# Kernel tuning notes

Hardware: AMD Instinct MI355X
Metric: run time of the kernel (lower is better)

Reference implementation:

```python
import jax, jax.numpy as jnp
import numpy as np

VOCAB = 100000
EMBED = 128
BATCH = 64
INPUT_LEN = 128
NB_WORDS = 50
RETAIN_P = 1.0  # dropout = 0.0


def setup_inputs() -> dict:
    key = jax.random.key(0)
    k1, k2 = jax.random.split(key)
    X = jax.random.randint(k1, (BATCH, INPUT_LEN, NB_WORDS), 0, VOCAB, dtype=jnp.int32)
    W = jax.random.normal(k2, (VOCAB, EMBED), dtype=jnp.float32)
    # original build() zeroes row 0 (padding row)
    W = W.at[0].set(0.0)
    return {"X": X, "W": W}


def reference(X, W):
    # inference path: B = ones(input_dim) * retain_p, so W_eff = W * retain_p
    # gather: (B, L, nb_words, E)
    emb = W[X] * RETAIN_P
    # zero-mask padding index 0, then bag-of-words sum over word axis
    mask = (X != 0).astype(emb.dtype)[..., None]
    out = jnp.sum(emb * mask, axis=2)  # (B, L, E)
    return out
```

## Files before the change

kernel.cpp:

```cpp
#include <hip/hip_runtime.h>
#include <hip/hip_bf16.h>


#define VOCAB     100000
#define EMBED     128
#define BATCH     64
#define INPUT_LEN 128
#define NB_WORDS  50
#define POSITIONS (BATCH * INPUT_LEN)

__global__ __launch_bounds__(256) void bag_embedding_kernel(
    const int* __restrict__ X,
    const float* __restrict__ W,
    float* __restrict__ out)
{
    const int gtid = blockIdx.x * blockDim.x + threadIdx.x;
    const int pos  = gtid >> 6;
    const int lane = threadIdx.x & 63;
    if (pos >= POSITIONS) return;

    const int* xp = X + pos * NB_WORDS;
    int myidx = (lane < NB_WORDS) ? xp[lane] : 0;

    const float2* __restrict__ W2 = (const float2*)W;
    float2 acc = make_float2(0.0f, 0.0f);

    #pragma unroll
    for (int w = 0; w < NB_WORDS; ++w) {
        int idx = __shfl(myidx, w);
        float2 v = W2[(size_t)idx * (EMBED / 2) + lane];
        acc.x += v.x;
        acc.y += v.y;
    }

    float2* o2 = (float2*)out;
    o2[(size_t)pos * (EMBED / 2) + lane] = acc;
}

extern "C" void kernel_launch(void* const* d_in, const int* in_sizes, int n_in,
                              void* d_out, int out_size, void* d_ws, size_t ws_size,
                              hipStream_t stream) {
    const int*   X = (const int*)d_in[0];
    const float* W = (const float*)d_in[1];
    float*     out = (float*)d_out;

    const int threads = 256;
    const int total   = POSITIONS * 64;
    const int blocks  = (total + threads - 1) / threads;
    bag_embedding_kernel<<<blocks, threads, 0, stream>>>(X, W, out);
}
```

Baseline: 104.6 us.

## Partition embedding gather by vocabulary range across blocks with a two-phase reduction

Splits the bag-of-words gather into 8 vocabulary ranges. Block index modulo 8 picks the range, so each block only gathers the rows of W whose indices fall inside its range and writes a partial sum to workspace. A second kernel sums the 8 partials into the output. The aim is to keep each group of blocks working on a smaller slice of W so the gathers hit in cache more often, which may line up with round-robin dispatch across XCDs. In exchange it adds about 64MB of workspace write and read traffic, a second kernel launch, and a serial ballot loop that has less memory-level parallelism than the fully unrolled loop.

```diff
diff --git a/kernel.cpp b/kernel.cpp
--- a/kernel.cpp
+++ b/kernel.cpp
@@ -8,8 +8,61 @@
 #define INPUT_LEN 128
 #define NB_WORDS  50
 #define POSITIONS (BATCH * INPUT_LEN)
+#define RANGES    8
+#define ROWS_PER_RANGE ((VOCAB + RANGES - 1) / RANGES)
 
-__global__ __launch_bounds__(256) void bag_embedding_kernel(
+__global__ __launch_bounds__(256) void bag_phase1(
+    const int* __restrict__ X,
+    const float* __restrict__ W,
+    float* __restrict__ ws)
+{
+    const int b     = blockIdx.x;
+    const int r     = b & (RANGES - 1);
+    const int chunk = b >> 3;
+    const int wave  = threadIdx.x >> 6;
+    const int lane  = threadIdx.x & 63;
+    const int pos   = chunk * 4 + wave;
+
+    const int lo = r * ROWS_PER_RANGE;
+    const int hi = (lo + ROWS_PER_RANGE < VOCAB) ? lo + ROWS_PER_RANGE : VOCAB;
+
+    const int* xp = X + pos * NB_WORDS;
+    int myidx = (lane < NB_WORDS) ? xp[lane] : -1;
+    bool inr = (lane < NB_WORDS) & (myidx >= lo) & (myidx < hi);
+    unsigned long long mask = __ballot(inr);
+
+    const float2* __restrict__ W2 = (const float2*)W;
+    float2 acc = make_float2(0.0f, 0.0f);
+
+    while (mask) {
+        int w = __ffsll((unsigned long long)mask) - 1;
+        mask &= mask - 1;
+        int idx = __builtin_amdgcn_readlane(myidx, w);
+        float2 v = W2[(size_t)idx * (EMBED / 2) + lane];
+        acc.x += v.x;
+        acc.y += v.y;
+    }
+
+    float2* o = (float2*)ws + ((size_t)r * POSITIONS + pos) * (EMBED / 2) + lane;
+    *o = acc;
+}
+
+__global__ __launch_bounds__(256) void bag_phase2(
+    const float* __restrict__ ws,
+    float* __restrict__ out)
+{
+    const int t = blockIdx.x * blockDim.x + threadIdx.x;
+    const float4* __restrict__ w4 = (const float4*)ws;
+    float4 s = make_float4(0.0f, 0.0f, 0.0f, 0.0f);
+    #pragma unroll
+    for (int r = 0; r < RANGES; ++r) {
+        float4 v = w4[(size_t)r * POSITIONS * (EMBED / 4) + t];
+        s.x += v.x; s.y += v.y; s.z += v.z; s.w += v.w;
+    }
+    ((float4*)out)[t] = s;
+}
+
+__global__ __launch_bounds__(256) void bag_onephase(
     const int* __restrict__ X,
     const float* __restrict__ W,
     float* __restrict__ out)
@@ -24,7 +77,6 @@
 
     const float2* __restrict__ W2 = (const float2*)W;
     float2 acc = make_float2(0.0f, 0.0f);
-
     #pragma unroll
     for (int w = 0; w < NB_WORDS; ++w) {
         int idx = __shfl(myidx, w);
@@ -32,7 +84,6 @@
         acc.x += v.x;
         acc.y += v.y;
     }
-
     float2* o2 = (float2*)out;
     o2[(size_t)pos * (EMBED / 2) + lane] = acc;
 }
@@ -44,8 +95,15 @@
     const float* W = (const float*)d_in[1];
     float*     out = (float*)d_out;
 
-    const int threads = 256;
-    const int total   = POSITIONS * 64;
-    const int blocks  = (total + threads - 1) / threads;
-    bag_embedding_kernel<<<blocks, threads, 0, stream>>>(X, W, out);
+    const size_t ws_needed = (size_t)RANGES * POSITIONS * EMBED * sizeof(float);
+    if (ws_size >= ws_needed) {
+        float* ws = (float*)d_ws;
+        bag_phase1<<<(POSITIONS / 4) * RANGES, 256, 0, stream>>>(X, W, ws);
+        bag_phase2<<<POSITIONS * (EMBED / 4) / 256, 256, 0, stream>>>(ws, out);
+    } else {
+        const int threads = 256;
+        const int total   = POSITIONS * 64;
+        const int blocks  = (total + threads - 1) / threads;
+        bag_onephase<<<blocks, threads, 0, stream>>>(X, W, out);
+    }
 }
```

After: 127.6 us. +22.0%, slower.

## Partition vocab into ranges per block for cache locality, reduce bf16 partials

Applied to the files above, without the earlier changes.

Splits the gather into two kernels. In the first, each block handles only words whose index falls in one of eight vocab ranges, aiming to keep that range's rows of W cache-resident, and it writes bf16-packed partial sums to a workspace. The second kernel sums the eight partials into fp32 output. This trades extra launches, the workspace traffic and bf16 rounding of the partials (a precision loss) for better reuse of W in cache. The new path runs only when the workspace is large enough, otherwise the old single-phase kernel is used.

```diff
diff --git a/kernel.cpp b/kernel.cpp
--- a/kernel.cpp
+++ b/kernel.cpp
@@ -1,5 +1,6 @@
 #include <hip/hip_runtime.h>
 #include <hip/hip_bf16.h>
+#include <stdint.h>
 
 
 #define VOCAB     100000
@@ -8,8 +9,77 @@
 #define INPUT_LEN 128
 #define NB_WORDS  50
 #define POSITIONS (BATCH * INPUT_LEN)
+#define RANGES    8
+#define ROWS_PER_RANGE (VOCAB / RANGES)
 
-__global__ __launch_bounds__(256) void bag_embedding_kernel(
+__device__ __forceinline__ uint32_t pack_bf16x2(float a, float b) {
+    uint32_t ua = __builtin_bit_cast(uint32_t, a);
+    uint32_t ub = __builtin_bit_cast(uint32_t, b);
+    uint32_t ra = (ua + 0x7fffu + ((ua >> 16) & 1u)) >> 16;
+    uint32_t rb = (ub + 0x7fffu + ((ub >> 16) & 1u)) >> 16;
+    return (rb << 16) | (ra & 0xffffu);
+}
+
+__global__ __launch_bounds__(256) void bag_phase1(
+    const int* __restrict__ X,
+    const float* __restrict__ W,
+    uint32_t* __restrict__ ws)
+{
+    const int b    = blockIdx.x;
+    const int r    = b & (RANGES - 1);
+    const int pos  = (b >> 3) * 4 + (threadIdx.x >> 6);
+    const int lane = threadIdx.x & 63;
+
+    const int lo = r * ROWS_PER_RANGE;
+    const int hi = lo + ROWS_PER_RANGE;
+
+    const int* xp = X + pos * NB_WORDS;
+    int myidx = (lane < NB_WORDS) ? xp[lane] : -1;
+    unsigned long long m = __ballot(myidx >= lo && myidx < hi);
+
+    const float2* __restrict__ W2 = (const float2*)W;
+    float2 acc = make_float2(0.0f, 0.0f);
+
+    while (m) {
+        int i0 = 0, i1 = 0, i2 = 0, i3 = 0;
+        {        int l = __ffsll(m) - 1; i0 = __builtin_amdgcn_readlane(myidx, l); m &= m - 1; }
+        if (m) { int l = __ffsll(m) - 1; i1 = __builtin_amdgcn_readlane(myidx, l); m &= m - 1; }
+        if (m) { int l = __ffsll(m) - 1; i2 = __builtin_amdgcn_readlane(myidx, l); m &= m - 1; }
+        if (m) { int l = __ffsll(m) - 1; i3 = __builtin_amdgcn_readlane(myidx, l); m &= m - 1; }
+        float2 v0 = W2[(size_t)i0 * (EMBED / 2) + lane];
+        float2 v1 = W2[(size_t)i1 * (EMBED / 2) + lane];
+        float2 v2 = W2[(size_t)i2 * (EMBED / 2) + lane];
+        float2 v3 = W2[(size_t)i3 * (EMBED / 2) + lane];
+        acc.x += v0.x + v1.x + v2.x + v3.x;
+        acc.y += v0.y + v1.y + v2.y + v3.y;
+    }
+
+    ws[((size_t)r * POSITIONS + pos) * (EMBED / 2) + lane] = pack_bf16x2(acc.x, acc.y);
+}
+
+__global__ __launch_bounds__(256) void bag_phase2(
+    const uint32_t* __restrict__ ws,
+    float* __restrict__ out)
+{
+    const int t = blockIdx.x * blockDim.x + threadIdx.x;
+    const uint4* __restrict__ w4 = (const uint4*)ws;
+    float s[8] = {0.f, 0.f, 0.f, 0.f, 0.f, 0.f, 0.f, 0.f};
+    #pragma unroll
+    for (int r = 0; r < RANGES; ++r) {
+        uint4 u = w4[(size_t)r * POSITIONS * (EMBED / 8) + t];
+        uint32_t ua[4] = {u.x, u.y, u.z, u.w};
+        #pragma unroll
+        for (int j = 0; j < 4; ++j) {
+            s[2 * j]     += __builtin_bit_cast(float, ua[j] << 16);
+            s[2 * j + 1] += __builtin_bit_cast(float, ua[j] & 0xffff0000u);
+        }
+    }
+    float4* o4 = (float4*)out;
+    o4[(size_t)t * 2]     = make_float4(s[0], s[1], s[2], s[3]);
+    o4[(size_t)t * 2 + 1] = make_float4(s[4], s[5], s[6], s[7]);
+}
+
+__global__ __launch_bounds__(256) void bag_onephase(
     const int* __restrict__ X,
     const float* __restrict__ W,
     float* __restrict__ out)
@@ -24,7 +94,6 @@
 
     const float2* __restrict__ W2 = (const float2*)W;
     float2 acc = make_float2(0.0f, 0.0f);
-
     #pragma unroll
     for (int w = 0; w < NB_WORDS; ++w) {
         int idx = __shfl(myidx, w);
@@ -32,7 +101,6 @@
         acc.x += v.x;
         acc.y += v.y;
     }
-
     float2* o2 = (float2*)out;
     o2[(size_t)pos * (EMBED / 2) + lane] = acc;
 }
@@ -44,8 +112,15 @@
     const float* W = (const float*)d_in[1];
     float*     out = (float*)d_out;
 
-    const int threads = 256;
-    const int total   = POSITIONS * 64;
-    const int blocks  = (total + threads - 1) / threads;
-    bag_embedding_kernel<<<blocks, threads, 0, stream>>>(X, W, out);
+    const size_t ws_needed = (size_t)RANGES * POSITIONS * (EMBED / 2) * 4;
+    if (ws_size >= ws_needed) {
+        uint32_t* ws = (uint32_t*)d_ws;
+        bag_phase1<<<(POSITIONS / 4) * RANGES, 256, 0, stream>>>(X, W, ws);
+        bag_phase2<<<POSITIONS * (EMBED / 8) / 256, 256, 0, stream>>>(ws, out);
+    } else {
+        const int threads = 256;
+        const int total   = POSITIONS * 64;
+        const int blocks  = (total + threads - 1) / threads;
+        bag_onephase<<<blocks, threads, 0, stream>>>(X, W, out);
+    }
 }
```

New measurement: 113.1 us. 8.1% more time.

## Convert embedding table to bf16 in workspace before gathering

Applied to the files above, without the earlier changes.

Adds a pre-pass that rounds the fp32 embedding table to bf16 (round to nearest even) in the workspace buffer. The gather kernel then reads 4-byte packed pairs instead of 8-byte float2 per lane, halving bytes per gathered row. The intent is to cut the random-gather traffic, which dominates the cost. In exchange it adds a full read and write pass over the table on every call and lowers numeric precision of the sums. It falls back to the original kernel if the workspace is too small.

```diff
diff --git a/kernel.cpp b/kernel.cpp
--- a/kernel.cpp
+++ b/kernel.cpp
@@ -1,5 +1,6 @@
 #include <hip/hip_runtime.h>
 #include <hip/hip_bf16.h>
+#include <stdint.h>
 
 
 #define VOCAB     100000
@@ -8,8 +9,56 @@
 #define INPUT_LEN 128
 #define NB_WORDS  50
 #define POSITIONS (BATCH * INPUT_LEN)
+#define W_ELEMS   (VOCAB * EMBED)
 
-__global__ __launch_bounds__(256) void bag_embedding_kernel(
+__device__ __forceinline__ uint32_t bf16_rne(float f) {
+    uint32_t u = __builtin_bit_cast(uint32_t, f);
+    return (u + 0x7fffu + ((u >> 16) & 1u)) >> 16;
+}
+
+__global__ __launch_bounds__(256) void w_to_bf16(
+    const float* __restrict__ W,
+    uint32_t* __restrict__ Wb)
+{
+    const int t = blockIdx.x * blockDim.x + threadIdx.x;
+    const float4* __restrict__ W4 = (const float4*)W;
+    float4 a = W4[(size_t)t * 2];
+    float4 b = W4[(size_t)t * 2 + 1];
+    uint4 o;
+    o.x = bf16_rne(a.x) | (bf16_rne(a.y) << 16);
+    o.y = bf16_rne(a.z) | (bf16_rne(a.w) << 16);
+    o.z = bf16_rne(b.x) | (bf16_rne(b.y) << 16);
+    o.w = bf16_rne(b.z) | (bf16_rne(b.w) << 16);
+    ((uint4*)Wb)[t] = o;
+}
+
+__global__ __launch_bounds__(256) void bag_gather_bf16(
+    const int* __restrict__ X,
+    const uint32_t* __restrict__ Wb,
+    float* __restrict__ out)
+{
+    const int gtid = blockIdx.x * blockDim.x + threadIdx.x;
+    const int pos  = gtid >> 6;
+    const int lane = threadIdx.x & 63;
+    if (pos >= POSITIONS) return;
+
+    const int* xp = X + pos * NB_WORDS;
+    int myidx = (lane < NB_WORDS) ? xp[lane] : 0;
+
+    float accx = 0.0f, accy = 0.0f;
+    #pragma unroll
+    for (int w = 0; w < NB_WORDS; ++w) {
+        int idx = __shfl(myidx, w);
+        uint32_t u = Wb[(size_t)idx * (EMBED / 2) + lane];
+        accx += __builtin_bit_cast(float, u << 16);
+        accy += __builtin_bit_cast(float, u & 0xffff0000u);
+    }
+
+    float2* o2 = (float2*)out;
+    o2[(size_t)pos * (EMBED / 2) + lane] = make_float2(accx, accy);
+}
+
+__global__ __launch_bounds__(256) void bag_onephase(
     const int* __restrict__ X,
     const float* __restrict__ W,
     float* __restrict__ out)
@@ -24,7 +73,6 @@
 
     const float2* __restrict__ W2 = (const float2*)W;
     float2 acc = make_float2(0.0f, 0.0f);
-
     #pragma unroll
     for (int w = 0; w < NB_WORDS; ++w) {
         int idx = __shfl(myidx, w);
@@ -32,7 +80,6 @@
         acc.x += v.x;
         acc.y += v.y;
     }
-
     float2* o2 = (float2*)out;
     o2[(size_t)pos * (EMBED / 2) + lane] = acc;
 }
@@ -44,8 +91,12 @@
     const float* W = (const float*)d_in[1];
     float*     out = (float*)d_out;
 
-    const int threads = 256;
-    const int total   = POSITIONS * 64;
-    const int blocks  = (total + threads - 1) / threads;
-    bag_embedding_kernel<<<blocks, threads, 0, stream>>>(X, W, out);
+    const size_t ws_needed = (size_t)W_ELEMS * 2;
+    if (ws_size >= ws_needed) {
+        uint32_t* Wb = (uint32_t*)d_ws;
+        w_to_bf16<<<W_ELEMS / 8 / 256, 256, 0, stream>>>(W, Wb);
+        bag_gather_bf16<<<POSITIONS * 64 / 256, 256, 0, stream>>>(X, Wb, out);
+    } else {
+        bag_onephase<<<POSITIONS * 64 / 256, 256, 0, stream>>>(X, W, out);
+    }
 }
```

Result: no change. 104.7 us (+0.1%).
